# Kernel optimization log

Hardware: AMD Instinct MI355X
Metric: run time of the kernel (lower is better)

## Reference

```python
import jax, jax.numpy as jnp
import numpy as np

KS = 2        # kernel_size
DIL = 1       # dilation
FILTERS = 512
Z_DIM = 128
B, C, T = 8, 512, 4096
TZ = T + 2 * (KS - 1)


def _conv1d(x, w, b):
    # x: (B, L, Cin), w: (ks, Cin, Cout) -> VALID conv, channels-last (keras Conv1D)
    y = jax.lax.conv_general_dilated(x, w, window_strides=(1,), padding='VALID',
                                     dimension_numbers=('NWC', 'WIO', 'NWC'))
    return y + b


def _adaptor(z, w1, b1, w2, b2):
    return _conv1d(jax.nn.relu(_conv1d(z, w1, b1)), w2, b2)


def setup_inputs() -> dict:
    key = jax.random.key(0)
    ks = jax.random.split(key, 10)
    lim = np.sqrt(6.0 / FILTERS)
    u = lambda k, shp: jax.random.uniform(k, shp, jnp.float32, -lim, lim)
    return {
        'x': jax.random.normal(ks[0], (B, C, T), jnp.float32),
        'z': jax.random.normal(ks[1], (B, TZ, Z_DIM), jnp.float32),
        'ww1': u(ks[2], (KS, Z_DIM, FILTERS)), 'wb1': jnp.zeros((FILTERS,), jnp.float32),
        'ww2': u(ks[3], (KS, FILTERS, FILTERS)), 'wb2': jnp.zeros((FILTERS,), jnp.float32),
        'bw1': u(ks[4], (KS, Z_DIM, FILTERS)), 'bb1': jnp.zeros((FILTERS,), jnp.float32),
        'bw2': u(ks[5], (KS, FILTERS, FILTERS)), 'bb2': jnp.zeros((FILTERS,), jnp.float32),
    }


def reference(x, z, ww1, wb1, ww2, wb2, bw1, bb1, bw2, bb2):
    m = x.shape[1]
    t = x.shape[2]
    pad = DIL * (KS - 1)
    xp = jnp.pad(x, ((0, 0), (0, 0), (0, pad)))
    end = t + pad
    # im2col-style unfold: (B, C*KS, T)
    xu = jnp.concatenate([xp[:, :, pad - i * DIL: end - i * DIL] for i in range(KS)], axis=1)
    weights = _adaptor(z, ww1, wb1, ww2, wb2)   # (B, T, F)
    bias = _adaptor(z, bw1, bb1, bw2, bb2)      # (B, T, F)
    y = jnp.matmul(xu, weights)                 # (B, C*KS, F)
    return y[:, :m, :] + bias[:, :m, :]
```

## Files before the change

kernel.cpp:

```cpp
#include <hip/hip_runtime.h>

typedef short short8 __attribute__((ext_vector_type(8)));
typedef float float4v __attribute__((ext_vector_type(4)));
typedef __attribute__((address_space(1))) const unsigned int gu32;
typedef __attribute__((address_space(3))) unsigned int lu32;

__device__ __forceinline__ unsigned short f2bf(float f) {
  unsigned int u = __builtin_bit_cast(unsigned int, f);
  u += 0x7FFFu + ((u >> 16) & 1u);
  return (unsigned short)(u >> 16);
}
__device__ __forceinline__ float bf2f(unsigned short s) {
  return __builtin_bit_cast(float, (unsigned int)s << 16);
}

__global__ __launch_bounds__(256) void prep_w(
    const float* __restrict__ ww1, const float* __restrict__ ww2,
    const float* __restrict__ bw1, const float* __restrict__ bw2,
    const float* __restrict__ z,
    unsigned short* __restrict__ w1T, unsigned short* __restrict__ w2T,
    unsigned short* __restrict__ b1T, unsigned short* __restrict__ b2T,
    unsigned short* __restrict__ zb)
{
  int i = blockIdx.x * 256 + threadIdx.x;
  if (i < 131072) {
    int n = i & 511, k = i >> 9;
    w1T[n * 256 + k] = f2bf(ww1[i]);
  } else if (i < 655360) {
    int j = i - 131072; int n = j & 511, k = j >> 9;
    w2T[n * 1024 + k] = f2bf(ww2[j]);
  } else if (i < 786432) {
    int j = i - 655360; int n = j & 511, k = j >> 9;
    b1T[n * 256 + k] = f2bf(bw1[j]);
  } else if (i < 1310720) {
    int j = i - 786432; int n = j & 511, k = j >> 9;
    b2T[n * 1024 + k] = f2bf(bw2[j]);
  } else {
    int j = i - 1310720;
    zb[j] = f2bf(z[j]);
  }
}

template<int BM, int BN, bool RELU, bool OBF16, bool TRANS, bool SPLITK, int NH,
         bool ROWPACK, bool DBUF>
__device__ __forceinline__ void gemm_core(
    int bx, int by, int bz, int nzTot, unsigned short* smem,
    const unsigned short* __restrict__ A,
    const unsigned short* __restrict__ A2,
    const unsigned short* __restrict__ Bt,
    const float* __restrict__ biasv,
    void* __restrict__ outp,
    void* __restrict__ outp2,
    int M, int Kchunk, int RPB, int EXTRA, int BSCALE,
    int nHalf, int bRowMask,
    long long bStrideB, long long outBatchStride, int outLd)
{
  constexpr int WM = BM / 2, WN = BN / 2;
  constexpr int NI = WM / 16, NJ = WN / 16;
  constexpr int AI = BM / 64;
  constexpr int BI = BN / 64;
  constexpr int SA1 = BM * 32, SB1 = BN * 32;
  unsigned short* sB0 = smem + NH * SA1;

  const int tid  = threadIdx.x;
  const int lane = tid & 63;
  const int wave = tid >> 6;
  const int wm = wave >> 1, wn = wave & 1;
  const int lr = lane & 15, quad = lane >> 4;

  const int r0 = bx * BM;
  const int n0 = by * BN;
  const int bb = r0 / RPB;
  const int Ktot = SPLITK ? Kchunk * nzTot : Kchunk;
  const int kOff = SPLITK ? bz * Kchunk : 0;
  const long long bOffB = (long long)bb * bStrideB;
  const unsigned short* Ae = (nHalf && n0 >= nHalf) ? A2 : A;

  const int srow = lane >> 2;
  const int sg = (lane & 3) ^ (srow & 3);
  const unsigned short* gA[AI]; unsigned short* ldsA[AI];
#pragma unroll
  for (int c = 0; c < AI; ++c) {
    int instr = c * 4 + wave;
    int row = instr * 16 + srow;
    int r = r0 + row; if (r > M - 1) r = M - 1;
    gA[c] = Ae + ((long long)r + (long long)(r / RPB) * EXTRA) * BSCALE + kOff + sg * 8;
    ldsA[c] = smem + instr * 512;
  }
  const unsigned short* gB[BI]; unsigned short* ldsB[BI];
#pragma unroll
  for (int c = 0; c < BI; ++c) {
    int instr = c * 4 + wave;
    int row = instr * 16 + srow;
    gB[c] = Bt + (long long)((n0 + row) & bRowMask) * Ktot + bOffB + kOff + sg * 8;
    ldsB[c] = sB0 + instr * 512;
  }

  int aoff[NI], boff[NJ];
#pragma unroll
  for (int i = 0; i < NI; ++i) {
    int rr = wm * WM + i * 16 + lr;
    aoff[i] = rr * 32 + ((quad ^ (rr & 3)) * 8);
  }
#pragma unroll
  for (int j = 0; j < NJ; ++j) {
    int rr = wn * WN + j * 16 + lr;
    boff[j] = rr * 32 + ((quad ^ (rr & 3)) * 8);
  }

  float4v acc[NI][NJ];
  const float4v z4 = {0.f, 0.f, 0.f, 0.f};
#pragma unroll
  for (int i = 0; i < NI; ++i)
#pragma unroll
    for (int j = 0; j < NJ; ++j) acc[i][j] = z4;

  if (DBUF) {
    auto stage_ch = [&](int kk, int h) {
#pragma unroll
      for (int c = 0; c < AI; ++c)
        __builtin_amdgcn_global_load_lds((gu32*)(gA[c] + kk),
                                         (lu32*)(ldsA[c] + h * SA1), 16, 0, 0);
#pragma unroll
      for (int c = 0; c < BI; ++c)
        __builtin_amdgcn_global_load_lds((gu32*)(gB[c] + kk),
                                         (lu32*)(ldsB[c] + h * SB1), 16, 0, 0);
    };
    stage_ch(0, 0);
    __syncthreads();
    int rbuf = 0;
    for (int k0 = 0; k0 < Kchunk; k0 += 32) {
      if (k0 + 32 < Kchunk) stage_ch(k0 + 32, rbuf ^ 1);
      short8 af[NI], bfr[NJ];
#pragma unroll
      for (int i = 0; i < NI; ++i) af[i] = *(const short8*)(smem + rbuf * SA1 + aoff[i]);
#pragma unroll
      for (int j = 0; j < NJ; ++j) bfr[j] = *(const short8*)(sB0 + rbuf * SB1 + boff[j]);
#pragma unroll
      for (int i = 0; i < NI; ++i)
#pragma unroll
        for (int j = 0; j < NJ; ++j)
          acc[i][j] = __builtin_amdgcn_mfma_f32_16x16x32_bf16(af[i], bfr[j], acc[i][j], 0, 0, 0);
      __syncthreads();
      rbuf ^= 1;
    }
  } else {
    for (int k0 = 0; k0 < Kchunk; k0 += 32 * NH) {
#pragma unroll
      for (int h = 0; h < NH; ++h) {
#pragma unroll
        for (int c = 0; c < AI; ++c)
          __builtin_amdgcn_global_load_lds((gu32*)(gA[c] + k0 + h * 32),
                                           (lu32*)(ldsA[c] + h * SA1), 16, 0, 0);
#pragma unroll
        for (int c = 0; c < BI; ++c)
          __builtin_amdgcn_global_load_lds((gu32*)(gB[c] + k0 + h * 32),
                                           (lu32*)(ldsB[c] + h * SB1), 16, 0, 0);
      }
      __syncthreads();
#pragma unroll
      for (int h = 0; h < NH; ++h) {
        short8 af[NI], bfr[NJ];
#pragma unroll
        for (int i = 0; i < NI; ++i) af[i] = *(const short8*)(smem + h * SA1 + aoff[i]);
#pragma unroll
        for (int j = 0; j < NJ; ++j) bfr[j] = *(const short8*)(sB0 + h * SB1 + boff[j]);
#pragma unroll
        for (int i = 0; i < NI; ++i)
#pragma unroll
          for (int j = 0; j < NJ; ++j)
            acc[i][j] = __builtin_amdgcn_mfma_f32_16x16x32_bf16(af[i], bfr[j], acc[i][j], 0, 0, 0);
      }
      __syncthreads();
    }
  }

  if (TRANS) {
    unsigned short* Ts = smem;
    const int t0l = r0 - bb * RPB;
#pragma unroll
    for (int p = 0; p < 2; ++p) {
      if (wn == p) {
#pragma unroll
        for (int j = 0; j < NJ; ++j) {
          int frl = j * 16 + lr;
          float bv = biasv[n0 + p * WN + frl];
#pragma unroll
          for (int i = 0; i < NI; ++i) {
            int tr = wm * WM + i * 16 + quad * 4;
            unsigned long long pk = 0;
#pragma unroll
            for (int g = 0; g < 4; ++g) {
              float vv = acc[i][j][g] + bv;
              if (RELU) vv = fmaxf(vv, 0.f);
              pk |= (unsigned long long)f2bf(vv) << (16 * g);
            }
            *(unsigned long long*)(Ts + frl * (BM + 8) + tr) = pk;
          }
        }
      }
      __syncthreads();
      int frl = tid >> 2, sgg = tid & 3;
      unsigned short* dst = (unsigned short*)outp + (long long)bb * outBatchStride
                          + (long long)(n0 + p * WN + frl) * outLd + t0l + sgg * (BM / 4);
      const unsigned short* srcp = Ts + frl * (BM + 8) + sgg * (BM / 4);
#pragma unroll
      for (int u = 0; u < BM / 32; ++u)
        *(uint4*)(dst + u * 8) = *(const uint4*)(srcp + u * 8);
      __syncthreads();
    }
  } else if (ROWPACK) {
    constexpr int P  = (BM > 64) ? 2 : 1;
    constexpr int RP = BM / P;
    constexpr int BNP = BN + 8;
    constexpr int TPR = 256 / RP;
    constexpr int EPT = BN / TPR;
    void* op = (SPLITK && bz) ? outp2 : outp;
    unsigned short* R = smem;
#pragma unroll
    for (int p = 0; p < P; ++p) {
      if (P == 1 || wm == p) {
#pragma unroll
        for (int j = 0; j < NJ; ++j) {
          int cc = wn * WN + j * 16 + lr;
#pragma unroll
          for (int i = 0; i < NI; ++i) {
            int rl = (P == 1 ? wm * WM : 0) + i * 16 + quad * 4;
#pragma unroll
            for (int g = 0; g < 4; ++g)
              R[(rl + g) * BNP + cc] = f2bf(acc[i][j][g]);
          }
        }
      }
      __syncthreads();
      int rloc = tid / TPR, part = tid % TPR;
      unsigned short* dstp = (unsigned short*)op
                           + (long long)(r0 + p * RP + rloc) * outLd + n0 + part * EPT;
      const unsigned short* srcp = R + rloc * BNP + part * EPT;
#pragma unroll
      for (int u = 0; u < EPT / 8; ++u)
        *(uint4*)(dstp + u * 8) = *(const uint4*)(srcp + u * 8);
      if (p + 1 < P) __syncthreads();
    }
  } else {
    void* op = (SPLITK && bz) ? outp2 : outp;
#pragma unroll
    for (int j = 0; j < NJ; ++j) {
      int n_g = n0 + wn * WN + j * 16 + lr;
      float bv = biasv ? biasv[n_g] : 0.f;
#pragma unroll
      for (int i = 0; i < NI; ++i) {
        int r_base = r0 + wm * WM + i * 16 + quad * 4;
#pragma unroll
        for (int g = 0; g < 4; ++g) {
          int r_g = r_base + g;
          if (r_g >= M) continue;
          float v = acc[i][j][g] + bv;
          if (RELU) v = fmaxf(v, 0.f);
          long long oidx = (long long)r_g * outLd + n_g;
          if (OBF16) ((unsigned short*)op)[oidx] = f2bf(v);
          else       ((float*)op)[oidx] = v;
        }
      }
    }
  }
}

template<int BM, int BN, bool RELU, bool OBF16, bool TRANS, bool SPLITK, int NH,
         bool ROWPACK, bool DBUF>
__global__ __launch_bounds__(256)
void gemm_bt(const unsigned short* __restrict__ A,
             const unsigned short* __restrict__ A2,
             const unsigned short* __restrict__ Bt,
             const float* __restrict__ biasv,
             void* __restrict__ outp,
             void* __restrict__ outp2,
             int M, int Kchunk, int RPB, int EXTRA, int BSCALE,
             int nHalf, int bRowMask,
             long long bStrideB, long long outBatchStride, int outLd)
{
  constexpr int STAGE = NH * (BM * 32 + BN * 32);
  constexpr int REPK = TRANS ? (BN / 2) * (BM + 8)
                     : (ROWPACK ? (BM > 64 ? (BM / 2) * (BN + 8) : BM * (BN + 8)) : 0);
  constexpr int SMEMN = (REPK > STAGE) ? REPK : STAGE;
  __shared__ unsigned short smem[SMEMN];
  gemm_core<BM, BN, RELU, OBF16, TRANS, SPLITK, NH, ROWPACK, DBUF>(
      blockIdx.x, blockIdx.y, blockIdx.z, gridDim.z, smem,
      A, A2, Bt, biasv, outp, outp2,
      M, Kchunk, RPB, EXTRA, BSCALE, nHalf, bRowMask,
      bStrideB, outBatchStride, outLd);
}

__global__ __launch_bounds__(256) void mega(
    const float* __restrict__ x,
    const unsigned short* __restrict__ zb,
    const unsigned short* __restrict__ w1T,
    const unsigned short* __restrict__ b1T,
    const float* __restrict__ wb1,
    const float* __restrict__ bb1,
    unsigned short* __restrict__ h1T,
    unsigned short* __restrict__ h1b,
    unsigned short* __restrict__ xs,
    unsigned short* __restrict__ xz,
    float* __restrict__ rs)
{
  __shared__ unsigned short smem[8704];
  int b = blockIdx.x;
  if (b < 1024) {
    gemm_core<128, 128, true, true, true, false, 1, false, false>(
        b & 255, b >> 8, 0, 1, smem,
        zb, nullptr, w1T, wb1, h1T, nullptr,
        32768, 256, 4096, 2, 128, 0, 0xFFFF, 0, 512ll * 4096, 4096);
  } else if (b < 1284) {
    int idx = b - 1024;
    gemm_core<64, 128, true, true, false, false, 1, false, false>(
        idx % 65, idx / 65, 0, 1, smem,
        zb, nullptr, b1T, bb1, h1b, nullptr,
        4104, 256, 513, 3585, 128, 0, 0xFFFF, 0, 0, 512);
  } else {
    float* red = (float*)smem;
    long long r = b - 1284;
    const float* xr = x + r * 4096;
    int t0 = threadIdx.x * 16;
    float v[17];
    const float4* xr4 = (const float4*)(xr + t0);
#pragma unroll
    for (int q = 0; q < 4; ++q) {
      float4 f = xr4[q];
      v[q * 4] = f.x; v[q * 4 + 1] = f.y; v[q * 4 + 2] = f.z; v[q * 4 + 3] = f.w;
    }
    v[16] = (t0 + 16 < 4096) ? xr[t0 + 16] : 0.f;
    unsigned int spk[8], zpk[8];
    float sum = 0.f;
#pragma unroll
    for (int q = 0; q < 8; ++q) {
      unsigned short s0 = f2bf(v[2 * q + 1]);
      unsigned short s1 = f2bf(v[2 * q + 2]);
      sum += bf2f(s0);
      sum += bf2f(s1);
      spk[q] = (unsigned int)s0 | ((unsigned int)s1 << 16);
      unsigned short z0 = (t0 == 0 && q == 0) ? (unsigned short)0 : f2bf(v[2 * q]);
      unsigned short z1 = f2bf(v[2 * q + 1]);
      zpk[q] = (unsigned int)z0 | ((unsigned int)z1 << 16);
    }
    *(uint4*)(xs + r * 4096 + t0)     = *(uint4*)(spk);
    *(uint4*)(xs + r * 4096 + t0 + 8) = *(uint4*)(spk + 4);
    *(uint4*)(xz + r * 4096 + t0)     = *(uint4*)(zpk);
    *(uint4*)(xz + r * 4096 + t0 + 8) = *(uint4*)(zpk + 4);
#pragma unroll
    for (int off = 32; off > 0; off >>= 1) sum += __shfl_down(sum, off);
    if ((threadIdx.x & 63) == 0) red[threadIdx.x >> 6] = sum;
    __syncthreads();
    if (threadIdx.x == 0) rs[r] = red[0] + red[1] + red[2] + red[3];
  }
}

__global__ __launch_bounds__(256) void final_gemm3(
    const unsigned short* __restrict__ p0,
    const unsigned short* __restrict__ p1,
    const unsigned short* __restrict__ h1b,
    const unsigned short* __restrict__ w2T,
    const unsigned short* __restrict__ b2T,
    const float* __restrict__ rs,
    const float* __restrict__ wb2,
    const float* __restrict__ bb2,
    float* __restrict__ out)
{
  constexpr int SA1 = 64 * 32, SB1 = 64 * 32;
  __shared__ unsigned short smem[4 * SA1 + 4 * SB1];
  const int tid = threadIdx.x;
  const int lane = tid & 63, wave = tid >> 6;
  const int wm = wave >> 1, wn = wave & 1;
  const int lr = lane & 15, quad = lane >> 4;
  const int r0 = blockIdx.x * 64, n0 = blockIdx.y * 64;

  const int srow = lane >> 2;
  const int sg = (lane & 3) ^ (srow & 3);
  const int row = wave * 16 + srow;
  const int rA = r0 + row;
  const int rB = n0 + row;
  const unsigned short* aP[3] = {
    p0 + (long long)rA * 1024 + sg * 8,
    p1 + (long long)rA * 1024 + sg * 8,
    h1b + ((long long)rA + (rA >> 9)) * 512 + sg * 8 };
  const unsigned short* bP[3] = {
    w2T + (long long)rB * 1024 + sg * 8,
    w2T + (long long)rB * 1024 + sg * 8,
    b2T + (long long)rB * 1024 + sg * 8 };
  unsigned short* ldsA = smem + wave * 512;
  unsigned short* ldsB = smem + 4 * SA1 + wave * 512;

  int aoff[2], boff[2];
#pragma unroll
  for (int i = 0; i < 2; ++i) {
    int rr = wm * 32 + i * 16 + lr;
    aoff[i] = rr * 32 + ((quad ^ (rr & 3)) * 8);
    int nn = wn * 32 + i * 16 + lr;
    boff[i] = 4 * SA1 + nn * 32 + ((quad ^ (nn & 3)) * 8);
  }

  float4v acc[2][2];
  const float4v z4 = {0.f, 0.f, 0.f, 0.f};
  acc[0][0] = z4; acc[0][1] = z4; acc[1][0] = z4; acc[1][1] = z4;

  auto stg = [&](int k, int s) {
    int seg = k >> 10, kk = k & 1023;
    __builtin_amdgcn_global_load_lds((gu32*)(aP[seg] + kk), (lu32*)(ldsA + s * SA1), 16, 0, 0);
    __builtin_amdgcn_global_load_lds((gu32*)(bP[seg] + kk), (lu32*)(ldsB + s * SB1), 16, 0, 0);
  };
  stg(0, 0); stg(32, 1);
  __syncthreads();
  int rb = 0;
  for (int k0 = 0; k0 < 3072; k0 += 64) {
    if (k0 + 64 < 3072) { stg(k0 + 64, (rb ^ 1) * 2); stg(k0 + 96, (rb ^ 1) * 2 + 1); }
#pragma unroll
    for (int h = 0; h < 2; ++h) {
      int s = rb * 2 + h;
      short8 af[2], bfr[2];
      af[0] = *(const short8*)(smem + s * SA1 + aoff[0]);
      af[1] = *(const short8*)(smem + s * SA1 + aoff[1]);
      bfr[0] = *(const short8*)(smem + s * SB1 + boff[0]);
      bfr[1] = *(const short8*)(smem + s * SB1 + boff[1]);
#pragma unroll
      for (int i = 0; i < 2; ++i)
#pragma unroll
        for (int j = 0; j < 2; ++j)
          acc[i][j] = __builtin_amdgcn_mfma_f32_16x16x32_bf16(af[i], bfr[j], acc[i][j], 0, 0, 0);
    }
    __syncthreads();
    rb ^= 1;
  }

#pragma unroll
  for (int j = 0; j < 2; ++j) {
    int n_g = n0 + wn * 32 + j * 16 + lr;
    float w2b = wb2[n_g], bbv = bb2[n_g];
#pragma unroll
    for (int i = 0; i < 2; ++i) {
      int rb2 = r0 + wm * 32 + i * 16 + quad * 4;
#pragma unroll
      for (int g = 0; g < 4; ++g) {
        int r_g = rb2 + g;
        out[(long long)r_g * 512 + n_g] = acc[i][j][g] + rs[r_g] * w2b + bbv;
      }
    }
  }
}

extern "C" void kernel_launch(void* const* d_in, const int* in_sizes, int n_in,
                              void* d_out, int out_size, void* d_ws, size_t ws_size,
                              hipStream_t stream) {
  const float* x   = (const float*)d_in[0];
  const float* z   = (const float*)d_in[1];
  const float* ww1 = (const float*)d_in[2];
  const float* wb1 = (const float*)d_in[3];
  const float* ww2 = (const float*)d_in[4];
  const float* wb2 = (const float*)d_in[5];
  const float* bw1 = (const float*)d_in[6];
  const float* bb1 = (const float*)d_in[7];
  const float* bw2 = (const float*)d_in[8];
  const float* bb2 = (const float*)d_in[9];

  char* ws = (char*)d_ws;
  unsigned short* xs  = (unsigned short*)ws; ws += 16777216ll * 2;
  unsigned short* xz  = (unsigned short*)ws; ws += 16777216ll * 2;
  unsigned short* zb  = (unsigned short*)ws; ws += 4196352ll  * 2;
  unsigned short* h1T = (unsigned short*)ws; ws += 16777216ll * 2;
  unsigned short* h1b = (unsigned short*)ws; ws += 2101248ll  * 2;
  unsigned short* w2T = (unsigned short*)ws; ws += 524288ll * 2;
  unsigned short* b2T = (unsigned short*)ws; ws += 524288ll * 2;
  float* rs = (float*)ws;                    ws += 4096ll * 4;
  char* tail = ws;
  unsigned short* w1T = (unsigned short*)tail;
  unsigned short* b1T = (unsigned short*)tail + 131072;
  unsigned short* p0  = zb;
  unsigned short* p1  = (unsigned short*)tail;

  prep_w<<<21512, 256, 0, stream>>>(ww1, ww2, bw1, bw2, z, w1T, w2T, b1T, b2T, zb);
  mega<<<5380, 256, 0, stream>>>(x, zb, w1T, b1T, wb1, bb1, h1T, h1b, xs, xz, rs);
  gemm_bt<128, 128, false, true, false, true, 2, true, true><<<dim3(32, 8, 2), 256, 0, stream>>>(
      xs, xz, h1T, nullptr, p0, p1,
      4096, 2048, 512, 0, 4096, 512, 511, 512ll * 4096, 0, 1024);
  final_gemm3<<<dim3(64, 8), 256, 0, stream>>>(
      p0, p1, h1b, w2T, b2T, rs, wb2, bb2, (float*)d_out);
}
```

Measured before the change: 252.8 us.

## Use triple-buffered LDS pipeline with vmcnt waits, remap grid, interleave mega blocks

New measurement: 248.6 us. Within noise of the previous version (-1.7%).

```diff
diff --git a/kernel.cpp b/kernel.cpp
--- a/kernel.cpp
+++ b/kernel.cpp
@@ -60,6 +60,7 @@
   constexpr int AI = BM / 64;
   constexpr int BI = BN / 64;
   constexpr int SA1 = BM * 32, SB1 = BN * 32;
+  static_assert(!DBUF || (AI + BI == 4), "vmcnt immediates assume 4 glds/stage");
   unsigned short* sB0 = smem + NH * SA1;
 
   const int tid  = threadIdx.x;
@@ -78,22 +79,20 @@
 
   const int srow = lane >> 2;
   const int sg = (lane & 3) ^ (srow & 3);
-  const unsigned short* gA[AI]; unsigned short* ldsA[AI];
+  const unsigned short* gA[AI];
 #pragma unroll
   for (int c = 0; c < AI; ++c) {
     int instr = c * 4 + wave;
     int row = instr * 16 + srow;
     int r = r0 + row; if (r > M - 1) r = M - 1;
     gA[c] = Ae + ((long long)r + (long long)(r / RPB) * EXTRA) * BSCALE + kOff + sg * 8;
-    ldsA[c] = smem + instr * 512;
-  }
-  const unsigned short* gB[BI]; unsigned short* ldsB[BI];
+  }
+  const unsigned short* gB[BI];
 #pragma unroll
   for (int c = 0; c < BI; ++c) {
     int instr = c * 4 + wave;
     int row = instr * 16 + srow;
     gB[c] = Bt + (long long)((n0 + row) & bRowMask) * Ktot + bOffB + kOff + sg * 8;
-    ldsB[c] = sB0 + instr * 512;
   }
 
   int aoff[NI], boff[NJ];
@@ -116,34 +115,43 @@
     for (int j = 0; j < NJ; ++j) acc[i][j] = z4;
 
   if (DBUF) {
-    auto stage_ch = [&](int kk, int h) {
+    constexpr int RS = SA1 + SB1;
+    const int NT = Kchunk >> 5;
+    auto stg = [&](int t, int m) {
+      unsigned short* rb = smem + m * RS;
+      int kk = t * 32;
 #pragma unroll
       for (int c = 0; c < AI; ++c)
         __builtin_amdgcn_global_load_lds((gu32*)(gA[c] + kk),
-                                         (lu32*)(ldsA[c] + h * SA1), 16, 0, 0);
+                                         (lu32*)(rb + (c * 4 + wave) * 512), 16, 0, 0);
 #pragma unroll
       for (int c = 0; c < BI; ++c)
         __builtin_amdgcn_global_load_lds((gu32*)(gB[c] + kk),
-                                         (lu32*)(ldsB[c] + h * SB1), 16, 0, 0);
+                                         (lu32*)(rb + SA1 + (c * 4 + wave) * 512), 16, 0, 0);
     };
-    stage_ch(0, 0);
-    __syncthreads();
-    int rbuf = 0;
-    for (int k0 = 0; k0 < Kchunk; k0 += 32) {
-      if (k0 + 32 < Kchunk) stage_ch(k0 + 32, rbuf ^ 1);
+    stg(0, 0); stg(1, 1);
+    int m = 0;
+    for (int t = 0; t < NT; ++t) {
+      if (t + 1 < NT) asm volatile("s_waitcnt vmcnt(4)" ::: "memory");
+      else            asm volatile("s_waitcnt vmcnt(0)" ::: "memory");
+      __builtin_amdgcn_s_barrier();
+      __builtin_amdgcn_sched_barrier(0);
+      int m2 = m + 2; if (m2 >= 3) m2 -= 3;
+      if (t + 2 < NT) stg(t + 2, m2);
+      const unsigned short* rb = smem + m * RS;
       short8 af[NI], bfr[NJ];
 #pragma unroll
-      for (int i = 0; i < NI; ++i) af[i] = *(const short8*)(smem + rbuf * SA1 + aoff[i]);
-#pragma unroll
-      for (int j = 0; j < NJ; ++j) bfr[j] = *(const short8*)(sB0 + rbuf * SB1 + boff[j]);
+      for (int i = 0; i < NI; ++i) af[i] = *(const short8*)(rb + aoff[i]);
+#pragma unroll
+      for (int j = 0; j < NJ; ++j) bfr[j] = *(const short8*)(rb + SA1 + boff[j]);
 #pragma unroll
       for (int i = 0; i < NI; ++i)
 #pragma unroll
         for (int j = 0; j < NJ; ++j)
           acc[i][j] = __builtin_amdgcn_mfma_f32_16x16x32_bf16(af[i], bfr[j], acc[i][j], 0, 0, 0);
-      __syncthreads();
-      rbuf ^= 1;
-    }
+      if (++m == 3) m = 0;
+    }
+    __syncthreads();
   } else {
     for (int k0 = 0; k0 < Kchunk; k0 += 32 * NH) {
 #pragma unroll
@@ -151,11 +159,11 @@
 #pragma unroll
         for (int c = 0; c < AI; ++c)
           __builtin_amdgcn_global_load_lds((gu32*)(gA[c] + k0 + h * 32),
-                                           (lu32*)(ldsA[c] + h * SA1), 16, 0, 0);
+                                           (lu32*)(smem + (c * 4 + wave) * 512 + h * SA1), 16, 0, 0);
 #pragma unroll
         for (int c = 0; c < BI; ++c)
           __builtin_amdgcn_global_load_lds((gu32*)(gB[c] + k0 + h * 32),
-                                           (lu32*)(ldsB[c] + h * SB1), 16, 0, 0);
+                                           (lu32*)(sB0 + (c * 4 + wave) * 512 + h * SB1), 16, 0, 0);
       }
       __syncthreads();
 #pragma unroll
@@ -267,7 +275,7 @@
 }
 
 template<int BM, int BN, bool RELU, bool OBF16, bool TRANS, bool SPLITK, int NH,
-         bool ROWPACK, bool DBUF>
+         bool ROWPACK, bool DBUF, bool REMAP8>
 __global__ __launch_bounds__(256)
 void gemm_bt(const unsigned short* __restrict__ A,
              const unsigned short* __restrict__ A2,
@@ -279,13 +287,24 @@
              int nHalf, int bRowMask,
              long long bStrideB, long long outBatchStride, int outLd)
 {
-  constexpr int STAGE = NH * (BM * 32 + BN * 32);
+  constexpr int STAGE = DBUF ? 3 * (BM * 32 + BN * 32) : NH * (BM * 32 + BN * 32);
   constexpr int REPK = TRANS ? (BN / 2) * (BM + 8)
                      : (ROWPACK ? (BM > 64 ? (BM / 2) * (BN + 8) : BM * (BN + 8)) : 0);
   constexpr int SMEMN = (REPK > STAGE) ? REPK : STAGE;
   __shared__ unsigned short smem[SMEMN];
+  int bx, by, bz, nz;
+  if (REMAP8) {
+    int lin = blockIdx.x;
+    by = lin & 7;
+    int pos = lin >> 3;
+    bz = pos >> 5;
+    bx = pos & 31;
+    nz = 2;
+  } else {
+    bx = blockIdx.x; by = blockIdx.y; bz = blockIdx.z; nz = gridDim.z;
+  }
   gemm_core<BM, BN, RELU, OBF16, TRANS, SPLITK, NH, ROWPACK, DBUF>(
-      blockIdx.x, blockIdx.y, blockIdx.z, gridDim.z, smem,
+      bx, by, bz, nz, smem,
       A, A2, Bt, biasv, outp, outp2,
       M, Kchunk, RPB, EXTRA, BSCALE, nHalf, bRowMask,
       bStrideB, outBatchStride, outLd);
@@ -306,20 +325,24 @@
 {
   __shared__ unsigned short smem[8704];
   int b = blockIdx.x;
-  if (b < 1024) {
-    gemm_core<128, 128, true, true, true, false, 1, false, false>(
-        b & 255, b >> 8, 0, 1, smem,
-        zb, nullptr, w1T, wb1, h1T, nullptr,
-        32768, 256, 4096, 2, 128, 0, 0xFFFF, 0, 512ll * 4096, 4096);
-  } else if (b < 1284) {
-    int idx = b - 1024;
-    gemm_core<64, 128, true, true, false, false, 1, false, false>(
-        idx % 65, idx / 65, 0, 1, smem,
-        zb, nullptr, b1T, bb1, h1b, nullptr,
-        4104, 256, 513, 3585, 128, 0, 0xFFFF, 0, 0, 512);
+  int g = (b * 1284) / 5380;
+  bool isg = (((b + 1) * 1284) / 5380) > g;
+  if (isg) {
+    if (g < 1024) {
+      gemm_core<128, 128, true, true, true, false, 1, false, false>(
+          g & 255, g >> 8, 0, 1, smem,
+          zb, nullptr, w1T, wb1, h1T, nullptr,
+          32768, 256, 4096, 2, 128, 0, 0xFFFF, 0, 512ll * 4096, 4096);
+    } else {
+      int idx = g - 1024;
+      gemm_core<64, 128, true, true, false, false, 1, false, false>(
+          idx % 65, idx / 65, 0, 1, smem,
+          zb, nullptr, b1T, bb1, h1b, nullptr,
+          4104, 256, 513, 3585, 128, 0, 0xFFFF, 0, 0, 512);
+    }
   } else {
     float* red = (float*)smem;
-    long long r = b - 1284;
+    long long r = b - g;
     const float* xr = x + r * 4096;
     int t0 = threadIdx.x * 16;
     float v[17];
@@ -366,8 +389,8 @@
     const float* __restrict__ bb2,
     float* __restrict__ out)
 {
-  constexpr int SA1 = 64 * 32, SB1 = 64 * 32;
-  __shared__ unsigned short smem[4 * SA1 + 4 * SB1];
+  constexpr int RS = 8192;
+  __shared__ unsigned short smem[3 * RS];
   const int tid = threadIdx.x;
   const int lane = tid & 63, wave = tid >> 6;
   const int wm = wave >> 1, wn = wave & 1;
@@ -387,8 +410,6 @@
     w2T + (long long)rB * 1024 + sg * 8,
     w2T + (long long)rB * 1024 + sg * 8,
     b2T + (long long)rB * 1024 + sg * 8 };
-  unsigned short* ldsA = smem + wave * 512;
-  unsigned short* ldsB = smem + 4 * SA1 + wave * 512;
 
   int aoff[2], boff[2];
 #pragma unroll
@@ -396,39 +417,46 @@
     int rr = wm * 32 + i * 16 + lr;
     aoff[i] = rr * 32 + ((quad ^ (rr & 3)) * 8);
     int nn = wn * 32 + i * 16 + lr;
-    boff[i] = 4 * SA1 + nn * 32 + ((quad ^ (nn & 3)) * 8);
+    boff[i] = nn * 32 + ((quad ^ (nn & 3)) * 8);
   }
 
   float4v acc[2][2];
   const float4v z4 = {0.f, 0.f, 0.f, 0.f};
   acc[0][0] = z4; acc[0][1] = z4; acc[1][0] = z4; acc[1][1] = z4;
 
-  auto stg = [&](int k, int s) {
-    int seg = k >> 10, kk = k & 1023;
-    __builtin_amdgcn_global_load_lds((gu32*)(aP[seg] + kk), (lu32*)(ldsA + s * SA1), 16, 0, 0);
-    __builtin_amdgcn_global_load_lds((gu32*)(bP[seg] + kk), (lu32*)(ldsB + s * SB1), 16, 0, 0);
+  const int wslot = wave * 512;
+  auto stg = [&](int t, int m) {
+    int k = t * 64; int seg = k >> 10; int kk = k & 1023;
+    unsigned short* base = smem + m * RS;
+    __builtin_amdgcn_global_load_lds((gu32*)(aP[seg] + kk),      (lu32*)(base + wslot), 16, 0, 0);
+    __builtin_amdgcn_global_load_lds((gu32*)(aP[seg] + kk + 32), (lu32*)(base + 2048 + wslot), 16, 0, 0);
+    __builtin_amdgcn_global_load_lds((gu32*)(bP[seg] + kk),      (lu32*)(base + 4096 + wslot), 16, 0, 0);
+    __builtin_amdgcn_global_load_lds((gu32*)(bP[seg] + kk + 32), (lu32*)(base + 6144 + wslot), 16, 0, 0);
   };
-  stg(0, 0); stg(32, 1);
-  __syncthreads();
-  int rb = 0;
-  for (int k0 = 0; k0 < 3072; k0 += 64) {
-    if (k0 + 64 < 3072) { stg(k0 + 64, (rb ^ 1) * 2); stg(k0 + 96, (rb ^ 1) * 2 + 1); }
+  stg(0, 0); stg(1, 1);
+  int m = 0;
+  for (int t = 0; t < 48; ++t) {
+    if (t < 47) asm volatile("s_waitcnt vmcnt(4)" ::: "memory");
+    else        asm volatile("s_waitcnt vmcnt(0)" ::: "memory");
+    __builtin_amdgcn_s_barrier();
+    __builtin_amdgcn_sched_barrier(0);
+    int m2 = m + 2; if (m2 >= 3) m2 -= 3;
+    if (t + 2 < 48) stg(t + 2, m2);
+    const unsigned short* base = smem + m * RS;
 #pragma unroll
     for (int h = 0; h < 2; ++h) {
-      int s = rb * 2 + h;
       short8 af[2], bfr[2];
-      af[0] = *(const short8*)(smem + s * SA1 + aoff[0]);
-      af[1] = *(const short8*)(smem + s * SA1 + aoff[1]);
-      bfr[0] = *(const short8*)(smem + s * SB1 + boff[0]);
-      bfr[1] = *(const short8*)(smem + s * SB1 + boff[1]);
+      af[0] = *(const short8*)(base + h * 2048 + aoff[0]);
+      af[1] = *(const short8*)(base + h * 2048 + aoff[1]);
+      bfr[0] = *(const short8*)(base + 4096 + h * 2048 + boff[0]);
+      bfr[1] = *(const short8*)(base + 4096 + h * 2048 + boff[1]);
 #pragma unroll
       for (int i = 0; i < 2; ++i)
 #pragma unroll
         for (int j = 0; j < 2; ++j)
           acc[i][j] = __builtin_amdgcn_mfma_f32_16x16x32_bf16(af[i], bfr[j], acc[i][j], 0, 0, 0);
     }
-    __syncthreads();
-    rb ^= 1;
+    if (++m == 3) m = 0;
   }
 
 #pragma unroll
@@ -478,7 +506,7 @@
 
   prep_w<<<21512, 256, 0, stream>>>(ww1, ww2, bw1, bw2, z, w1T, w2T, b1T, b2T, zb);
   mega<<<5380, 256, 0, stream>>>(x, zb, w1T, b1T, wb1, bb1, h1T, h1b, xs, xz, rs);
-  gemm_bt<128, 128, false, true, false, true, 2, true, true><<<dim3(32, 8, 2), 256, 0, stream>>>(
+  gemm_bt<128, 128, false, true, false, true, 1, true, true, true><<<512, 256, 0, stream>>>(
       xs, xz, h1T, nullptr, p0, p1,
       4096, 2048, 512, 0, 4096, 512, 511, 512ll * 4096, 0, 1024);
   final_gemm3<<<dim3(64, 8), 256, 0, stream>>>(
```
